# Kernel tuning notes

Hardware: AMD Instinct MI355X
Metric: run time of the kernel (lower is better)

## Reference

```python
import jax, jax.numpy as jnp
import numpy as np

N_DIM = 1024
N_HEAD = 16
HEAD_DIM = N_DIM // N_HEAD


def setup_inputs() -> dict:
    key = jax.random.key(0)
    ks = jax.random.split(key, 9)
    B, S, D = 4, 2048, N_DIM
    std = 1.0 / np.sqrt(D)
    x = jax.random.normal(ks[0], (B, S, D), dtype=jnp.float32)
    w_q = jax.random.uniform(ks[1], (D, D), jnp.float32, -std, std)
    b_q = jax.random.uniform(ks[2], (D,), jnp.float32, -std, std)
    w_k = jax.random.uniform(ks[3], (D, D), jnp.float32, -std, std)
    b_k = jax.random.uniform(ks[4], (D,), jnp.float32, -std, std)
    w_v = jax.random.uniform(ks[5], (D, D), jnp.float32, -std, std)
    b_v = jax.random.uniform(ks[6], (D,), jnp.float32, -std, std)
    w_o = jax.random.uniform(ks[7], (D, D), jnp.float32, -std, std)
    b_o = jax.random.uniform(ks[8], (D,), jnp.float32, -std, std)
    return {"x": x, "w_q": w_q, "b_q": b_q, "w_k": w_k, "b_k": b_k,
            "w_v": w_v, "b_v": b_v, "w_o": w_o, "b_o": b_o}


def _split_heads(t, B, S):
    # [B,S,D] -> [B,H,S,hd]
    return t.reshape(B, S, N_HEAD, HEAD_DIM).transpose(0, 2, 1, 3)


def reference(x, w_q, b_q, w_k, b_k, w_v, b_v, w_o, b_o):
    B, S, D = x.shape
    q = _split_heads(x @ w_q.T + b_q, B, S)
    k = _split_heads(x @ w_k.T + b_k, B, S)
    v = _split_heads(x @ w_v.T + b_v, B, S)
    scale = 1.0 / np.sqrt(HEAD_DIM).astype(np.float32)
    # [B,H,S,S] scores (note: original's masked_fill is a no-op, so no masking)
    scores = jnp.einsum('bhqd,bhkd->bhqk', q, k) * scale
    probs = jax.nn.softmax(scores, axis=-1)
    out = jnp.einsum('bhqk,bhkd->bhqd', probs, v)
    concat = out.transpose(0, 2, 1, 3).reshape(B, S, D)
    return concat @ w_o.T + b_o
```

## Files before the change

### kernel.cpp

```cpp
#include <hip/hip_runtime.h>
#include <hip/hip_bf16.h>

typedef __bf16 bf16_t;
typedef __bf16 bf16x2 __attribute__((ext_vector_type(2)));
typedef __bf16 bf16x4 __attribute__((ext_vector_type(4)));
typedef __bf16 bf16x8 __attribute__((ext_vector_type(8)));
typedef float f32x4 __attribute__((ext_vector_type(4)));
typedef float f32x16 __attribute__((ext_vector_type(16)));
typedef unsigned int u32;
typedef u32 u32x4 __attribute__((ext_vector_type(4)));

#define MFMA16(a, b, c) __builtin_amdgcn_mfma_f32_16x16x32_bf16((a), (b), (c), 0, 0, 0)
#define MFMA32(a, b, c) __builtin_amdgcn_mfma_f32_32x32x16_bf16((a), (b), (c), 0, 0, 0)

__device__ __forceinline__ void gload_lds16(const bf16_t* g, bf16_t* l) {
    __builtin_amdgcn_global_load_lds((const __attribute__((address_space(1))) void*)g,
                                     (__attribute__((address_space(3))) void*)l, 16, 0, 0);
}

__device__ __forceinline__ u32 pack2(float a, float b) {
    bf16x2 t;
    t[0] = (bf16_t)a;
    t[1] = (bf16_t)b;
    return __builtin_bit_cast(u32, t);
}

__global__ __launch_bounds__(256)
void cvt_f32_bf16(const float* __restrict__ src, bf16_t* __restrict__ dst, int n8) {
    int i = blockIdx.x * 256 + threadIdx.x;
    if (i >= n8) return;
    const float4* s = (const float4*)src;
    float4 a = s[i * 2], b = s[i * 2 + 1];
    bf16x8 o;
    o[0] = (bf16_t)a.x; o[1] = (bf16_t)a.y; o[2] = (bf16_t)a.z; o[3] = (bf16_t)a.w;
    o[4] = (bf16_t)b.x; o[5] = (bf16_t)b.y; o[6] = (bf16_t)b.z; o[7] = (bf16_t)b.w;
    ((bf16x8*)dst)[i] = o;
}

template <typename OutT>
__global__ __launch_bounds__(256)
void gemm_bias_nt(const bf16_t* __restrict__ A, const bf16_t* __restrict__ W,
                  const float* __restrict__ bias, OutT* __restrict__ C,
                  int M, int N, int K) {
    constexpr int BM = 128, BN = 128, BK = 32;
    __shared__ __align__(16) bf16_t As[BM * BK];
    __shared__ __align__(16) bf16_t Ws[BN * BK];
    const int tid = threadIdx.x;
    const int wid = tid >> 6;
    const int lane = tid & 63;
    const int l15 = lane & 15, lh = lane >> 4;
    const int wr = wid >> 1, wc = wid & 1;
    const int row0 = blockIdx.x * BM, col0 = blockIdx.y * BN;

    f32x4 acc[4][4] = {};

    for (int k0 = 0; k0 < K; k0 += BK) {
        #pragma unroll
        for (int p = 0; p < 2; ++p) {
            int c = p * 256 + tid;
            int r = c >> 2;
            int kc = (c & 3) * 8;
            gload_lds16(A + (size_t)(row0 + r) * K + k0 + kc, As + c * 8);
            gload_lds16(W + (size_t)(col0 + r) * K + k0 + kc, Ws + c * 8);
        }
        __syncthreads();
        bf16x8 af[4], bfr[4];
        #pragma unroll
        for (int mi = 0; mi < 4; ++mi)
            af[mi] = *(const bf16x8*)(As + (wr * 64 + mi * 16 + l15) * BK + lh * 8);
        #pragma unroll
        for (int ni = 0; ni < 4; ++ni)
            bfr[ni] = *(const bf16x8*)(Ws + (wc * 64 + ni * 16 + l15) * BK + lh * 8);
        #pragma unroll
        for (int mi = 0; mi < 4; ++mi)
            #pragma unroll
            for (int ni = 0; ni < 4; ++ni)
                acc[mi][ni] = MFMA16(af[mi], bfr[ni], acc[mi][ni]);
        __syncthreads();
    }

    #pragma unroll
    for (int ni = 0; ni < 4; ++ni) {
        int col = col0 + wc * 64 + ni * 16 + l15;
        float bv = bias[col];
        #pragma unroll
        for (int mi = 0; mi < 4; ++mi) {
            #pragma unroll
            for (int r = 0; r < 4; ++r) {
                int row = row0 + wr * 64 + mi * 16 + lh * 4 + r;
                C[(size_t)row * N + col] = (OutT)(acc[mi][ni][r] + bv);
            }
        }
    }
}

__global__ __launch_bounds__(512)
void flash_attn(const bf16_t* __restrict__ Q, const bf16_t* __restrict__ Kg,
                const bf16_t* __restrict__ Vg, bf16_t* __restrict__ O,
                int S, int ldqkv) {
    constexpr int HD = 64, KVB = 64, OD = 1024;
    const int wkid = (blockIdx.x & 7) * 64 + (blockIdx.x >> 3);
    const int qt = wkid & 7;
    const int bh = wkid >> 3;
    const int b = bh >> 4, h = bh & 15;
    const int tid = threadIdx.x, w = tid >> 6, lane = tid & 63;
    const int l31 = lane & 31, hi = lane >> 5;
    const size_t rowbase = (size_t)b * S;
    const int hc = h * HD;

    __shared__ __align__(16) bf16_t Ks[2][64 * 64];
    __shared__ __align__(16) bf16_t Vt[2][64 * 64];

    const int q0 = qt * 256 + w * 32;
    bf16x8 qf[4];
    {
        const bf16_t* qp = Q + (rowbase + q0 + l31) * ldqkv + hc + hi * 8;
        #pragma unroll
        for (int t = 0; t < 4; ++t) {
            bf16x8 v = *(const bf16x8*)(qp + t * 16);
            #pragma unroll
            for (int j = 0; j < 8; ++j) v[j] = (bf16_t)((float)v[j] * 0.125f);
            qf[t] = v;
        }
    }

    const int kdst = w * 512;
    const bf16_t* kgsrc;
    {
        int chunk = w * 64 + lane;
        int kk = chunk >> 3, c = chunk & 7;
        kgsrc = Kg + (rowbase + kk) * ldqkv + hc + ((c ^ (kk & 7)) * 8);
    }

    const int kp = tid & 31, dbase = (tid >> 5) * 4;
    const bf16_t* vsrc0 = Vg + (rowbase + 2 * kp) * ldqkv + hc + dbase;
    const bf16_t* vsrc1 = Vg + (rowbase + 2 * kp + 1) * ldqkv + hc + dbase;

    f32x16 oacc0 = {}, oacc1 = {};
    float l_run = 0.f;

    auto stageK = [&](int bufn, int kv) {
        gload_lds16(kgsrc + (size_t)kv * ldqkv, &Ks[bufn][kdst]);
    };
    auto writeVT = [&](int bufn, bf16x4 a, bf16x4 bvec) {
        #pragma unroll
        for (int j = 0; j < 4; ++j) {
            int d = dbase + j;
            u32 pk = (u32)__builtin_bit_cast(unsigned short, (bf16_t)a[j]) |
                     ((u32)__builtin_bit_cast(unsigned short, (bf16_t)bvec[j]) << 16);
            *(u32*)&Vt[bufn][d * 64 + (((kp >> 2) ^ (d & 7)) * 8) + (kp & 3) * 2] = pk;
        }
    };

    stageK(0, 0);
    {
        bf16x4 a = *(const bf16x4*)vsrc0;
        bf16x4 bv = *(const bf16x4*)vsrc1;
        writeVT(0, a, bv);
    }
    __syncthreads();

    int cur = 0;
    const int NIT = S / KVB;
    for (int it = 0; it < NIT; ++it) {
        const bool pre = (it < NIT - 1);
        bf16x4 va, vb;
        if (pre) {
            size_t off = (size_t)(it + 1) * KVB * ldqkv;
            va = *(const bf16x4*)(vsrc0 + off);
            vb = *(const bf16x4*)(vsrc1 + off);
            stageK(cur ^ 1, (it + 1) * KVB);
        }

        f32x16 sf0 = {}, sf1 = {};
        const int kswz = l31 & 7;
        #pragma unroll
        for (int t = 0; t < 4; ++t) {
            bf16x8 ka0 = *(const bf16x8*)&Ks[cur][l31 * 64 + (((t * 2 + hi) ^ kswz) * 8)];
            bf16x8 ka1 = *(const bf16x8*)&Ks[cur][(32 + l31) * 64 + (((t * 2 + hi) ^ kswz) * 8)];
            sf0 = MFMA32(ka0, qf[t], sf0);
            sf1 = MFMA32(ka1, qf[t], sf1);
        }

        float p[32];
        #pragma unroll
        for (int i = 0; i < 16; ++i) {
            p[i] = __expf(sf0[i]);
            p[16 + i] = __expf(sf1[i]);
        }
        float e8[8];
        #pragma unroll
        for (int i = 0; i < 8; ++i)
            e8[i] = (p[i] + p[i + 8]) + (p[i + 16] + p[i + 24]);
        float s = ((e8[0] + e8[1]) + (e8[2] + e8[3])) + ((e8[4] + e8[5]) + (e8[6] + e8[7]));
        s += __shfl_xor(s, 32);
        l_run += s;

        if (pre) writeVT(cur ^ 1, va, vb);

        #pragma unroll
        for (int kt = 0; kt < 4; ++kt) {
            const int base = (kt >> 1) * 16 + (kt & 1) * 8;
            u32 X = pack2(p[base + 0], p[base + 1]);
            u32 Y = pack2(p[base + 4], p[base + 5]);
            asm volatile("v_permlane32_swap_b32 %0, %1" : "+v"(X), "+v"(Y));
            u32 Z = pack2(p[base + 2], p[base + 3]);
            u32 W = pack2(p[base + 6], p[base + 7]);
            asm volatile("v_permlane32_swap_b32 %0, %1" : "+v"(Z), "+v"(W));
            u32x4 fw; fw.x = X; fw.y = Z; fw.z = Y; fw.w = W;
            bf16x8 pf = __builtin_bit_cast(bf16x8, fw);
            bf16x8 va0 = *(const bf16x8*)&Vt[cur][l31 * 64 + (((kt * 2 + hi) ^ kswz) * 8)];
            bf16x8 va1 = *(const bf16x8*)&Vt[cur][(32 + l31) * 64 + (((kt * 2 + hi) ^ kswz) * 8)];
            oacc0 = MFMA32(va0, pf, oacc0);
            oacc1 = MFMA32(va1, pf, oacc1);
        }

        __syncthreads();
        cur ^= 1;
    }

    float inv = 1.f / l_run;
    bf16_t* orow = O + (rowbase + q0 + l31) * OD + hc;
    #pragma unroll
    for (int g = 0; g < 4; ++g) {
        bf16x4 o0, o1;
        #pragma unroll
        for (int e = 0; e < 4; ++e) {
            o0[e] = (bf16_t)(oacc0[g * 4 + e] * inv);
            o1[e] = (bf16_t)(oacc1[g * 4 + e] * inv);
        }
        *(bf16x4*)(orow + g * 8 + hi * 4) = o0;
        *(bf16x4*)(orow + 32 + g * 8 + hi * 4) = o1;
    }
}

extern "C" void kernel_launch(void* const* d_in, const int* in_sizes, int n_in,
                              void* d_out, int out_size, void* d_ws, size_t ws_size,
                              hipStream_t stream) {
    const float* x   = (const float*)d_in[0];
    const float* w_q = (const float*)d_in[1];
    const float* b_q = (const float*)d_in[2];
    const float* w_k = (const float*)d_in[3];
    const float* b_k = (const float*)d_in[4];
    const float* w_v = (const float*)d_in[5];
    const float* b_v = (const float*)d_in[6];
    const float* w_o = (const float*)d_in[7];
    const float* b_o = (const float*)d_in[8];
    float* out = (float*)d_out;

    const int B = 4, S = 2048, D = 1024;
    const int M = B * S;
    const size_t MD = (size_t)M * D;
    const size_t DD = (size_t)D * D;

    bf16_t* xb   = (bf16_t*)d_ws;
    bf16_t* wqb  = xb + MD;
    bf16_t* wkb  = wqb + DD;
    bf16_t* wvb  = wkb + DD;
    bf16_t* wob  = wvb + DD;
    bf16_t* qkv  = wob + DD;
    bf16_t* cc   = qkv + (size_t)M * 3072;
    float*  bias_pack = (float*)(cc + MD);

    hipMemcpyAsync(bias_pack,       b_q, D * sizeof(float), hipMemcpyDeviceToDevice, stream);
    hipMemcpyAsync(bias_pack + D,   b_k, D * sizeof(float), hipMemcpyDeviceToDevice, stream);
    hipMemcpyAsync(bias_pack + 2*D, b_v, D * sizeof(float), hipMemcpyDeviceToDevice, stream);

    cvt_f32_bf16<<<(int)(MD / 8 / 256), 256, 0, stream>>>(x, xb, (int)(MD / 8));
    cvt_f32_bf16<<<(int)(DD / 8 / 256), 256, 0, stream>>>(w_q, wqb, (int)(DD / 8));
    cvt_f32_bf16<<<(int)(DD / 8 / 256), 256, 0, stream>>>(w_k, wkb, (int)(DD / 8));
    cvt_f32_bf16<<<(int)(DD / 8 / 256), 256, 0, stream>>>(w_v, wvb, (int)(DD / 8));
    cvt_f32_bf16<<<(int)(DD / 8 / 256), 256, 0, stream>>>(w_o, wob, (int)(DD / 8));

    dim3 bgq(M / 128, 3072 / 128);
    gemm_bias_nt<bf16_t><<<bgq, 256, 0, stream>>>(xb, wqb, bias_pack, qkv, M, 3072, D);

    flash_attn<<<dim3(512), 512, 0, stream>>>(qkv, qkv + D, qkv + 2 * D, cc, S, 3072);

    dim3 bgo(M / 128, D / 128);
    gemm_bias_nt<float><<<bgo, 256, 0, stream>>>(cc, wob, b_o, out, M, D, D);
}
```

Before: 226.5 us.

## Use 4-stage LDS pipelined GEMM with 256x128 tiles and 512 threads

Replaces the single-buffered GEMM with a 4-deep LDS ring buffer, prefetching three K-tiles ahead via direct global-to-LDS loads and manual vmcnt waits with one barrier per iteration. It also doubles the M tile to 256 with 8 waves per block. This targets the exposed global load latency and the double barrier per K step in both projection GEMMs. It relies on hand-written waitcnt counts matching the loads issued, uses more LDS, and halves the grid size.

```diff
diff --git a/kernel.cpp b/kernel.cpp
--- a/kernel.cpp
+++ b/kernel.cpp
@@ -38,45 +38,63 @@
 }
 
 template <typename OutT>
-__global__ __launch_bounds__(256)
-void gemm_bias_nt(const bf16_t* __restrict__ A, const bf16_t* __restrict__ W,
-                  const float* __restrict__ bias, OutT* __restrict__ C,
-                  int M, int N, int K) {
-    constexpr int BM = 128, BN = 128, BK = 32;
-    __shared__ __align__(16) bf16_t As[BM * BK];
-    __shared__ __align__(16) bf16_t Ws[BN * BK];
+__global__ __launch_bounds__(512)
+void gemm_bias_nt2(const bf16_t* __restrict__ A, const bf16_t* __restrict__ W,
+                   const float* __restrict__ bias, OutT* __restrict__ C,
+                   int M, int N, int K) {
+    constexpr int BM = 256, BN = 128, BK = 32;
+    __shared__ __align__(16) bf16_t Ab[4][BM * BK];
+    __shared__ __align__(16) bf16_t Bb[4][BN * BK];
     const int tid = threadIdx.x;
-    const int wid = tid >> 6;
+    const int w = tid >> 6;
     const int lane = tid & 63;
     const int l15 = lane & 15, lh = lane >> 4;
-    const int wr = wid >> 1, wc = wid & 1;
+    const int wr = w >> 1, wc = w & 1;
     const int row0 = blockIdx.x * BM, col0 = blockIdx.y * BN;
 
+    const int cA0 = tid;
+    const int cA1 = tid + 512;
+    const int cB  = tid;
+    const bf16_t* a0 = A + (size_t)(row0 + (cA0 >> 2)) * K + (cA0 & 3) * 8;
+    const bf16_t* a1 = A + (size_t)(row0 + (cA1 >> 2)) * K + (cA1 & 3) * 8;
+    const bf16_t* b0 = W + (size_t)(col0 + (cB >> 2)) * K + (cB & 3) * 8;
+
     f32x4 acc[4][4] = {};
-
-    for (int k0 = 0; k0 < K; k0 += BK) {
-        #pragma unroll
-        for (int p = 0; p < 2; ++p) {
-            int c = p * 256 + tid;
-            int r = c >> 2;
-            int kc = (c & 3) * 8;
-            gload_lds16(A + (size_t)(row0 + r) * K + k0 + kc, As + c * 8);
-            gload_lds16(W + (size_t)(col0 + r) * K + k0 + kc, Ws + c * 8);
-        }
-        __syncthreads();
+    const int NT = K / BK;
+
+    auto stage = [&](int t) {
+        bf16_t* base = &Ab[t & 3][0];
+        gload_lds16(a0 + (size_t)t * BK, base + cA0 * 8);
+        gload_lds16(a1 + (size_t)t * BK, base + cA1 * 8);
+        gload_lds16(b0 + (size_t)t * BK, &Bb[t & 3][0] + cB * 8);
+    };
+
+    stage(0); stage(1); stage(2);
+
+    for (int t = 0; t < NT; ++t) {
+        if (t < NT - 2)
+            asm volatile("s_waitcnt vmcnt(6)\n\ts_barrier" ::: "memory");
+        else if (t == NT - 2)
+            asm volatile("s_waitcnt vmcnt(3)\n\ts_barrier" ::: "memory");
+        else
+            asm volatile("s_waitcnt vmcnt(0)\n\ts_barrier" ::: "memory");
+
+        if (t + 3 < NT) stage(t + 3);
+
+        const bf16_t* ab = &Ab[t & 3][0];
+        const bf16_t* bb = &Bb[t & 3][0];
         bf16x8 af[4], bfr[4];
         #pragma unroll
         for (int mi = 0; mi < 4; ++mi)
-            af[mi] = *(const bf16x8*)(As + (wr * 64 + mi * 16 + l15) * BK + lh * 8);
+            af[mi] = *(const bf16x8*)(ab + (wr * 64 + mi * 16 + l15) * BK + lh * 8);
         #pragma unroll
         for (int ni = 0; ni < 4; ++ni)
-            bfr[ni] = *(const bf16x8*)(Ws + (wc * 64 + ni * 16 + l15) * BK + lh * 8);
+            bfr[ni] = *(const bf16x8*)(bb + (wc * 64 + ni * 16 + l15) * BK + lh * 8);
         #pragma unroll
         for (int mi = 0; mi < 4; ++mi)
             #pragma unroll
             for (int ni = 0; ni < 4; ++ni)
                 acc[mi][ni] = MFMA16(af[mi], bfr[ni], acc[mi][ni]);
-        __syncthreads();
     }
 
     #pragma unroll
@@ -272,11 +290,11 @@
     cvt_f32_bf16<<<(int)(DD / 8 / 256), 256, 0, stream>>>(w_v, wvb, (int)(DD / 8));
     cvt_f32_bf16<<<(int)(DD / 8 / 256), 256, 0, stream>>>(w_o, wob, (int)(DD / 8));
 
-    dim3 bgq(M / 128, 3072 / 128);
-    gemm_bias_nt<bf16_t><<<bgq, 256, 0, stream>>>(xb, wqb, bias_pack, qkv, M, 3072, D);
+    dim3 bgq(M / 256, 3072 / 128);
+    gemm_bias_nt2<bf16_t><<<bgq, 512, 0, stream>>>(xb, wqb, bias_pack, qkv, M, 3072, D);
 
     flash_attn<<<dim3(512), 512, 0, stream>>>(qkv, qkv + D, qkv + 2 * D, cc, S, 3072);
 
-    dim3 bgo(M / 128, D / 128);
-    gemm_bias_nt<float><<<bgo, 256, 0, stream>>>(cc, wob, b_o, out, M, D, D);
-}
+    dim3 bgo(M / 256, D / 128);
+    gemm_bias_nt2<float><<<bgo, 512, 0, stream>>>(cc, wob, b_o, out, M, D, D);
+}
```

Measured after the change: 232.7 us. 2.7% more time.
